# Kernel tuning notes

Measured on AMD Instinct MI355X. Metric: run time of the kernel, lower is better.

## Reference

```python
import jax, jax.numpy as jnp
import numpy as np

B, S, D = 4, 4096, 2048
E, H, SPE = 64, 1024, 1
NUM_SLOTS = E * SPE
TEMP = 1.0


def setup_inputs() -> dict:
    key = jax.random.key(0)
    ks = jax.random.split(key, 6)
    x = jax.random.normal(ks[0], (B, S, D), dtype=jnp.float32)
    W_disp = jax.random.normal(ks[1], (NUM_SLOTS, D), dtype=jnp.float32) * 0.02
    # torch Linear default init ~ U(-1/sqrt(fan_in), 1/sqrt(fan_in))
    W1 = jax.random.uniform(ks[2], (E, H, D), jnp.float32, -1.0, 1.0) / np.sqrt(D)
    b1 = jax.random.uniform(ks[3], (E, H), jnp.float32, -1.0, 1.0) / np.sqrt(D)
    W2 = jax.random.uniform(ks[4], (E, D, H), jnp.float32, -1.0, 1.0) / np.sqrt(H)
    b2 = jax.random.uniform(ks[5], (E, D), jnp.float32, -1.0, 1.0) / np.sqrt(H)
    return {"x": x, "W_disp": W_disp, "W1": W1, "b1": b1, "W2": W2, "b2": b2}


def reference(x, W_disp, W1, b1, W2, b2):
    # eval mode: dropout inactive, no calibration, z_loss_weight=0
    Bb, Ss, Dd = x.shape
    xf = x.reshape(-1, Dd)                       # (T, D)
    logits = (xf @ W_disp.T) / TEMP              # (T, num_slots)
    dispatch = jax.nn.softmax(logits, axis=0)    # softmax over tokens (T > 1)
    combine = jax.nn.softmax(logits, axis=-1)    # softmax over slots
    slot_inputs = dispatch.T @ xf                # (num_slots, D)
    x_exp = slot_inputs.reshape(E, SPE, Dd)      # (E, S_per, D)
    h = jnp.einsum('esd,ehd->esh', x_exp, W1) + b1[:, None, :]
    h = jax.nn.gelu(h, approximate=False)        # torch F.gelu is exact (erf)
    out = jnp.einsum('esh,edh->esd', h, W2) + b2[:, None, :]
    slot_outputs = out.reshape(NUM_SLOTS, Dd)
    y = combine @ slot_outputs                   # (T, D)
    return y.reshape(Bb, Ss, Dd)
```

## Files before the change

kernel.cpp:

```cpp
#include <hip/hip_runtime.h>
#include <math.h>

#define T_TOK 16384
#define D_DIM 2048
#define NSLOT 64
#define H_DIM 1024
#define KSPLIT 8
#define KCH 256
#define TBLK 128

__global__ __launch_bounds__(256) void k_logits(const float* __restrict__ x,
                                                const float* __restrict__ Wd,
                                                float* __restrict__ plog,
                                                float* __restrict__ pz4) {
    __shared__ float xs[128][32];
    __shared__ float ws[64][32];
    const int tid = threadIdx.x;
    if (blockIdx.x == 0 && blockIdx.y == 0) pz4[tid] = 0.f;
    const int tblk = blockIdx.x * TBLK;
    const int koff = blockIdx.y * KCH;
    const int tq = tid >> 3;
    const int sg = tid & 7;
    float acc[4][8] = {};

    for (int kc = 0; kc < KCH; kc += 32) {
        __syncthreads();
        #pragma unroll
        for (int ii = 0; ii < 4; ++ii) {
            int fi = tid + ii * 256; int t = fi >> 3, c = fi & 7;
            *(float4*)&xs[t][(c ^ (t & 7)) << 2] =
                *(const float4*)&x[(size_t)(tblk + t) * D_DIM + koff + kc + c * 4];
        }
        #pragma unroll
        for (int ii = 0; ii < 2; ++ii) {
            int fi = tid + ii * 256; int s = fi >> 3, c = fi & 7;
            *(float4*)&ws[s][(c ^ (s & 7)) << 2] =
                *(const float4*)&Wd[(size_t)s * D_DIM + koff + kc + c * 4];
        }
        __syncthreads();
        #pragma unroll
        for (int c = 0; c < 8; ++c) {
            float4 wv[8];
            #pragma unroll
            for (int j = 0; j < 8; ++j)
                wv[j] = *(const float4*)&ws[sg + 8 * j][(c ^ sg) << 2];
            #pragma unroll
            for (int i = 0; i < 4; ++i) {
                float4 xv = *(const float4*)&xs[tq + 32 * i][(c ^ (tq & 7)) << 2];
                #pragma unroll
                for (int j = 0; j < 8; ++j)
                    acc[i][j] += xv.x * wv[j].x + xv.y * wv[j].y +
                                 xv.z * wv[j].z + xv.w * wv[j].w;
            }
        }
    }
    const size_t ksbase = (size_t)blockIdx.y * T_TOK;
    #pragma unroll
    for (int i = 0; i < 4; ++i)
        #pragma unroll
        for (int j = 0; j < 8; ++j)
            plog[(ksbase + tblk + tq + 32 * i) * NSLOT + sg + 8 * j] = acc[i][j];
}

__global__ __launch_bounds__(256) void k_lsum(const float* __restrict__ plog,
                                              float* __restrict__ elog,
                                              float* __restrict__ pz4) {
    __shared__ float zsh[4][64];
    const int tid = threadIdx.x;
    const int s = tid & 63, rq = tid >> 6;
    const int j0 = blockIdx.x * 32;
    float zacc = 0.f;
    #pragma unroll
    for (int i = 0; i < 8; ++i) {
        int r = j0 + rq * 8 + i;
        float v = 0.f;
        #pragma unroll
        for (int ks = 0; ks < KSPLIT; ++ks)
            v += plog[((size_t)ks * T_TOK + r) * NSLOT + s];
        float e = __expf(v);
        elog[(size_t)r * NSLOT + s] = e;
        zacc += e;
    }
    zsh[rq][s] = zacc;
    __syncthreads();
    if (tid < 64)
        atomicAdd(&pz4[(blockIdx.x & 3) * 64 + tid],
                  zsh[0][tid] + zsh[1][tid] + zsh[2][tid] + zsh[3][tid]);
}

__global__ __launch_bounds__(256) void k_slot(const float* __restrict__ x,
        const float* __restrict__ elog, float* __restrict__ partial) {
    __shared__ float xs[32][256];
    __shared__ float pls[32][64];
    const int tid = threadIdx.x;
    const int d0 = blockIdx.x * 256;
    const int tc0 = blockIdx.y * 256;
    const int dg = tid & 31, sgq = tid >> 5;
    float4 acc0[8] = {}, acc1[8] = {};

    for (int sub = 0; sub < 8; ++sub) {
        const int t0 = tc0 + sub * 32;
        __syncthreads();
        #pragma unroll
        for (int ii = 0; ii < 8; ++ii) {
            int fi = tid + ii * 256; int r = fi >> 6, c4 = fi & 63;
            *(float4*)&xs[r][c4 * 4] =
                *(const float4*)&x[(size_t)(t0 + r) * D_DIM + d0 + c4 * 4];
        }
        #pragma unroll
        for (int ii = 0; ii < 2; ++ii) {
            int fi = tid + ii * 256; int r = fi >> 4, s4 = fi & 15;
            *(float4*)&pls[r][s4 * 4] =
                *(const float4*)&elog[(size_t)(t0 + r) * NSLOT + s4 * 4];
        }
        __syncthreads();
        for (int t = 0; t < 32; ++t) {
            float4 xv0 = *(const float4*)&xs[t][dg * 4];
            float4 xv1 = *(const float4*)&xs[t][128 + dg * 4];
            #pragma unroll
            for (int i = 0; i < 8; ++i) {
                float p = pls[t][sgq * 8 + i];
                acc0[i].x += p * xv0.x; acc0[i].y += p * xv0.y;
                acc0[i].z += p * xv0.z; acc0[i].w += p * xv0.w;
                acc1[i].x += p * xv1.x; acc1[i].y += p * xv1.y;
                acc1[i].z += p * xv1.z; acc1[i].w += p * xv1.w;
            }
        }
    }
    #pragma unroll
    for (int i = 0; i < 8; ++i) {
        int s = sgq * 8 + i;
        *(float4*)&partial[((size_t)blockIdx.y * NSLOT + s) * D_DIM + d0 + dg * 4] = acc0[i];
        *(float4*)&partial[((size_t)blockIdx.y * NSLOT + s) * D_DIM + d0 + 128 + dg * 4] = acc1[i];
    }
}

__global__ __launch_bounds__(256) void k_sred(const float* __restrict__ partial,
                                              const float* __restrict__ pz4,
                                              float* __restrict__ slot_in) {
    const size_t idx = (size_t)blockIdx.x * 256 + threadIdx.x;
    const int s = (int)(idx >> 9);
    const float iz = 1.f / (pz4[s] + pz4[64 + s] + pz4[128 + s] + pz4[192 + s]);
    const float4* p4 = (const float4*)partial;
    float4 a = {0.f, 0.f, 0.f, 0.f};
    for (int c0 = 0; c0 < 8; ++c0) {
        float4 v[8];
        #pragma unroll
        for (int j = 0; j < 8; ++j)
            v[j] = p4[(size_t)(c0 * 8 + j) * (NSLOT * D_DIM / 4) + idx];
        #pragma unroll
        for (int j = 0; j < 8; ++j) {
            a.x += v[j].x; a.y += v[j].y; a.z += v[j].z; a.w += v[j].w;
        }
    }
    a.x *= iz; a.y *= iz; a.z *= iz; a.w *= iz;
    ((float4*)slot_in)[idx] = a;
}

__global__ __launch_bounds__(256) void k_mlp1(const float* __restrict__ W1,
                                              const float* __restrict__ b1,
                                              const float* __restrict__ slot_in,
                                              float* __restrict__ h) {
    const int wave = threadIdx.x >> 6, lane = threadIdx.x & 63;
    const int row = blockIdx.x * 4 + wave;
    const int e = row >> 10;
    const float* wr = W1 + (size_t)row * D_DIM;
    const float* xr = slot_in + (size_t)e * D_DIM;
    float acc = 0.f;
    #pragma unroll
    for (int i = 0; i < 8; ++i) {
        int k = (lane + i * 64) * 4;
        float4 w4 = *(const float4*)(wr + k);
        float4 x4 = *(const float4*)(xr + k);
        acc += w4.x * x4.x + w4.y * x4.y + w4.z * x4.z + w4.w * x4.w;
    }
    #pragma unroll
    for (int off = 32; off; off >>= 1) acc += __shfl_xor(acc, off);
    if (lane == 0) {
        float v = acc + b1[row];
        h[row] = 0.5f * v * (1.f + erff(v * 0.70710678118654752f));
    }
}

__global__ __launch_bounds__(256) void k_mlp2(const float* __restrict__ W2,
                                              const float* __restrict__ b2,
                                              const float* __restrict__ h,
                                              float* __restrict__ slot_out) {
    const int wave = threadIdx.x >> 6, lane = threadIdx.x & 63;
    const int row = blockIdx.x * 4 + wave;
    const int e = row >> 11;
    const float* wr = W2 + (size_t)row * H_DIM;
    const float* xr = h + (size_t)e * H_DIM;
    float acc = 0.f;
    #pragma unroll
    for (int i = 0; i < 4; ++i) {
        int k = (lane + i * 64) * 4;
        float4 w4 = *(const float4*)(wr + k);
        float4 x4 = *(const float4*)(xr + k);
        acc += w4.x * x4.x + w4.y * x4.y + w4.z * x4.z + w4.w * x4.w;
    }
    #pragma unroll
    for (int off = 32; off; off >>= 1) acc += __shfl_xor(acc, off);
    if (lane == 0) slot_out[row] = acc + b2[row];
}

__global__ __launch_bounds__(256) void k_combine(const float* __restrict__ elog,
                                                 const float* __restrict__ so,
                                                 float* __restrict__ y) {
    __shared__ float cl[128][68];
    __shared__ float sol[64][128];
    __shared__ float rinv[128];
    const int tid = threadIdx.x;
    const int d0 = blockIdx.x * 128;
    const int tb = blockIdx.y * 128;
    const int tq = tid >> 4;
    const int dgq = tid & 15;
    #pragma unroll
    for (int ii = 0; ii < 8; ++ii) {
        int fi = tid + ii * 256; int r = fi >> 4, s4 = fi & 15;
        *(float4*)&cl[r][s4 * 4] =
            *(const float4*)&elog[(size_t)(tb + r) * NSLOT + s4 * 4];
    }
    #pragma unroll
    for (int ii = 0; ii < 8; ++ii) {
        int fi = tid + ii * 256; int r = fi >> 5, c4 = fi & 31;
        *(float4*)&sol[r][c4 * 4] =
            *(const float4*)&so[(size_t)r * D_DIM + d0 + c4 * 4];
    }
    __syncthreads();
    if (tid < 128) {
        float zs = 0.f;
        #pragma unroll
        for (int q = 0; q < 16; ++q) {
            float4 v = *(const float4*)&cl[tid][q * 4];
            zs += v.x + v.y + v.z + v.w;
        }
        rinv[tid] = 1.f / zs;
    }
    __syncthreads();
    float4 acc0[8] = {}, acc1[8] = {};
    for (int s = 0; s < 64; ++s) {
        float4 sv0 = *(const float4*)&sol[s][dgq * 4];
        float4 sv1 = *(const float4*)&sol[s][64 + dgq * 4];
        #pragma unroll
        for (int i = 0; i < 8; ++i) {
            float cv = cl[tq + 16 * i][s];
            acc0[i].x += cv * sv0.x; acc0[i].y += cv * sv0.y;
            acc0[i].z += cv * sv0.z; acc0[i].w += cv * sv0.w;
            acc1[i].x += cv * sv1.x; acc1[i].y += cv * sv1.y;
            acc1[i].z += cv * sv1.z; acc1[i].w += cv * sv1.w;
        }
    }
    #pragma unroll
    for (int i = 0; i < 8; ++i) {
        float rz = rinv[tq + 16 * i];
        acc0[i].x *= rz; acc0[i].y *= rz; acc0[i].z *= rz; acc0[i].w *= rz;
        acc1[i].x *= rz; acc1[i].y *= rz; acc1[i].z *= rz; acc1[i].w *= rz;
        *(float4*)&y[(size_t)(tb + tq + 16 * i) * D_DIM + d0 + dgq * 4] = acc0[i];
        *(float4*)&y[(size_t)(tb + tq + 16 * i) * D_DIM + d0 + 64 + dgq * 4] = acc1[i];
    }
}

extern "C" void kernel_launch(void* const* d_in, const int* in_sizes, int n_in,
                              void* d_out, int out_size, void* d_ws, size_t ws_size,
                              hipStream_t stream) {
    const float* x  = (const float*)d_in[0];
    const float* Wd = (const float*)d_in[1];
    const float* W1 = (const float*)d_in[2];
    const float* b1 = (const float*)d_in[3];
    const float* W2 = (const float*)d_in[4];
    const float* b2 = (const float*)d_in[5];
    float* y = (float*)d_out;

    float* w = (float*)d_ws;
    float* plog     = w;
    float* elog     = plog + (size_t)KSPLIT * T_TOK * NSLOT;
    float* pz4      = elog + (size_t)T_TOK * NSLOT;
    float* partial  = pz4 + 256;
    float* slot_in  = partial + (size_t)64 * NSLOT * D_DIM;
    float* h        = slot_in + (size_t)NSLOT * D_DIM;
    float* slot_out = h + (size_t)NSLOT * H_DIM;

    k_logits<<<dim3(T_TOK / TBLK, KSPLIT), 256, 0, stream>>>(x, Wd, plog, pz4);
    k_lsum<<<512, 256, 0, stream>>>(plog, elog, pz4);
    k_slot<<<dim3(8, 64), 256, 0, stream>>>(x, elog, partial);
    k_sred<<<128, 256, 0, stream>>>(partial, pz4, slot_in);
    k_mlp1<<<(NSLOT * H_DIM) / 4, 256, 0, stream>>>(W1, b1, slot_in, h);
    k_mlp2<<<(NSLOT * D_DIM) / 4, 256, 0, stream>>>(W2, b2, h, slot_out);
    k_combine<<<dim3(16, 128), 256, 0, stream>>>(elog, slot_out, y);
}
```

Baseline: 446.9 us.

## Prefetch next tile into registers in logits and slot-reduction kernels

Both the logits GEMM and the slot-input accumulation kernels now load the next tile from global memory into registers while computing on the current shared-memory tile, then write it to shared memory after a barrier. The logits kernel also doubles its K chunk per stage to 64, which halves the number of stages. The aim is to hide global load latency behind FMA work. In exchange it raises register pressure and shared memory use, which may reduce occupancy.

```diff
diff --git a/kernel.cpp b/kernel.cpp
--- a/kernel.cpp
+++ b/kernel.cpp
@@ -13,8 +13,8 @@
                                                 const float* __restrict__ Wd,
                                                 float* __restrict__ plog,
                                                 float* __restrict__ pz4) {
-    __shared__ float xs[128][32];
-    __shared__ float ws[64][32];
+    __shared__ float xs[128 * 64];
+    __shared__ float ws[64 * 64];
     const int tid = threadIdx.x;
     if (blockIdx.x == 0 && blockIdx.y == 0) pz4[tid] = 0.f;
     const int tblk = blockIdx.x * TBLK;
@@ -22,38 +22,66 @@
     const int tq = tid >> 3;
     const int sg = tid & 7;
     float acc[4][8] = {};
-
-    for (int kc = 0; kc < KCH; kc += 32) {
-        __syncthreads();
-        #pragma unroll
-        for (int ii = 0; ii < 4; ++ii) {
-            int fi = tid + ii * 256; int t = fi >> 3, c = fi & 7;
-            *(float4*)&xs[t][(c ^ (t & 7)) << 2] =
-                *(const float4*)&x[(size_t)(tblk + t) * D_DIM + koff + kc + c * 4];
-        }
-        #pragma unroll
-        for (int ii = 0; ii < 2; ++ii) {
-            int fi = tid + ii * 256; int s = fi >> 3, c = fi & 7;
-            *(float4*)&ws[s][(c ^ (s & 7)) << 2] =
-                *(const float4*)&Wd[(size_t)s * D_DIM + koff + kc + c * 4];
-        }
-        __syncthreads();
-        #pragma unroll
-        for (int c = 0; c < 8; ++c) {
+    float4 px[8], pw[4];
+
+    const int xt = tid >> 4, xc = tid & 15;
+
+#define LOADSTAGE(KST)                                                        \
+    {                                                                         \
+        const int kb = koff + (KST) * 64;                                     \
+        _Pragma("unroll")                                                     \
+        for (int ii = 0; ii < 8; ++ii)                                        \
+            px[ii] = *(const float4*)&x[(size_t)(tblk + xt + ii * 16) * D_DIM \
+                                        + kb + xc * 4];                       \
+        _Pragma("unroll")                                                     \
+        for (int ii = 0; ii < 4; ++ii)                                        \
+            pw[ii] = *(const float4*)&Wd[(size_t)(xt + ii * 16) * D_DIM       \
+                                         + kb + xc * 4];                      \
+    }
+
+#define WRITESTAGE()                                                          \
+    {                                                                         \
+        _Pragma("unroll")                                                     \
+        for (int ii = 0; ii < 8; ++ii) {                                      \
+            int t = xt + ii * 16;                                             \
+            *(float4*)&xs[t * 64 + ((xc ^ (t & 7)) << 2)] = px[ii];           \
+        }                                                                     \
+        _Pragma("unroll")                                                     \
+        for (int ii = 0; ii < 4; ++ii) {                                      \
+            int s = xt + ii * 16;                                             \
+            *(float4*)&ws[s * 64 + ((xc ^ (s & 7)) << 2)] = pw[ii];           \
+        }                                                                     \
+    }
+
+    LOADSTAGE(0);
+    WRITESTAGE();
+    __syncthreads();
+    for (int kst = 0; kst < 4; ++kst) {
+        if (kst < 3) LOADSTAGE(kst + 1);
+        #pragma unroll
+        for (int c = 0; c < 16; ++c) {
             float4 wv[8];
             #pragma unroll
             for (int j = 0; j < 8; ++j)
-                wv[j] = *(const float4*)&ws[sg + 8 * j][(c ^ sg) << 2];
+                wv[j] = *(const float4*)&ws[(sg + 8 * j) * 64 + ((c ^ sg) << 2)];
             #pragma unroll
             for (int i = 0; i < 4; ++i) {
-                float4 xv = *(const float4*)&xs[tq + 32 * i][(c ^ (tq & 7)) << 2];
+                float4 xv = *(const float4*)&xs[(tq + 32 * i) * 64
+                                                + ((c ^ (tq & 7)) << 2)];
                 #pragma unroll
                 for (int j = 0; j < 8; ++j)
                     acc[i][j] += xv.x * wv[j].x + xv.y * wv[j].y +
                                  xv.z * wv[j].z + xv.w * wv[j].w;
             }
         }
-    }
+        if (kst < 3) {
+            __syncthreads();
+            WRITESTAGE();
+            __syncthreads();
+        }
+    }
+#undef LOADSTAGE
+#undef WRITESTAGE
     const size_t ksbase = (size_t)blockIdx.y * T_TOK;
     #pragma unroll
     for (int i = 0; i < 4; ++i)
@@ -96,24 +124,39 @@
     const int d0 = blockIdx.x * 256;
     const int tc0 = blockIdx.y * 256;
     const int dg = tid & 31, sgq = tid >> 5;
+    const int xr = tid >> 6, xc = tid & 63;
+    const int pr = tid >> 4, pc = tid & 15;
     float4 acc0[8] = {}, acc1[8] = {};
-
+    float4 gx[8], gp[2];
+
+#define SLOADSTAGE(SUB)                                                       \
+    {                                                                         \
+        const int t0 = tc0 + (SUB) * 32;                                      \
+        _Pragma("unroll")                                                     \
+        for (int ii = 0; ii < 8; ++ii)                                        \
+            gx[ii] = *(const float4*)&x[(size_t)(t0 + xr + ii * 4) * D_DIM    \
+                                        + d0 + xc * 4];                       \
+        _Pragma("unroll")                                                     \
+        for (int ii = 0; ii < 2; ++ii)                                        \
+            gp[ii] = *(const float4*)&elog[(size_t)(t0 + pr + ii * 16)        \
+                                           * NSLOT + pc * 4];                 \
+    }
+
+#define SWRITESTAGE()                                                         \
+    {                                                                         \
+        _Pragma("unroll")                                                     \
+        for (int ii = 0; ii < 8; ++ii)                                        \
+            *(float4*)&xs[xr + ii * 4][xc * 4] = gx[ii];                      \
+        _Pragma("unroll")                                                     \
+        for (int ii = 0; ii < 2; ++ii)                                        \
+            *(float4*)&pls[pr + ii * 16][pc * 4] = gp[ii];                    \
+    }
+
+    SLOADSTAGE(0);
+    SWRITESTAGE();
+    __syncthreads();
     for (int sub = 0; sub < 8; ++sub) {
-        const int t0 = tc0 + sub * 32;
-        __syncthreads();
-        #pragma unroll
-        for (int ii = 0; ii < 8; ++ii) {
-            int fi = tid + ii * 256; int r = fi >> 6, c4 = fi & 63;
-            *(float4*)&xs[r][c4 * 4] =
-                *(const float4*)&x[(size_t)(t0 + r) * D_DIM + d0 + c4 * 4];
-        }
-        #pragma unroll
-        for (int ii = 0; ii < 2; ++ii) {
-            int fi = tid + ii * 256; int r = fi >> 4, s4 = fi & 15;
-            *(float4*)&pls[r][s4 * 4] =
-                *(const float4*)&elog[(size_t)(t0 + r) * NSLOT + s4 * 4];
-        }
-        __syncthreads();
+        if (sub < 7) SLOADSTAGE(sub + 1);
         for (int t = 0; t < 32; ++t) {
             float4 xv0 = *(const float4*)&xs[t][dg * 4];
             float4 xv1 = *(const float4*)&xs[t][128 + dg * 4];
@@ -126,7 +169,14 @@
                 acc1[i].z += p * xv1.z; acc1[i].w += p * xv1.w;
             }
         }
-    }
+        if (sub < 7) {
+            __syncthreads();
+            SWRITESTAGE();
+            __syncthreads();
+        }
+    }
+#undef SLOADSTAGE
+#undef SWRITESTAGE
     #pragma unroll
     for (int i = 0; i < 8; ++i) {
         int s = sgq * 8 + i;
```

Result: slower. 1.053 ms (+135.7%).

## Rebalance grid sizes: split sred reduction, more lsum blocks, persistent-style MLP waves

Applied to the files above, without the earlier changes.

k_lsum now handles 16 rows per block with twice as many blocks, giving more parallelism. k_sred splits the 64-way partial reduction across four waves per block and finishes it in shared memory, raising the grid from 128 to 512 blocks so more CUs pull memory bandwidth. The MLP GEMV kernels switch to a fixed 2048-block grid, with each wave looping over rows strided by 8192, which cuts block launch overhead. The cost is an extra sync and a shared-memory step in sred, plus less latency hiding in the MLP kernels if too few waves stay resident.

```diff
diff --git a/kernel.cpp b/kernel.cpp
--- a/kernel.cpp
+++ b/kernel.cpp
@@ -68,11 +68,11 @@
     __shared__ float zsh[4][64];
     const int tid = threadIdx.x;
     const int s = tid & 63, rq = tid >> 6;
-    const int j0 = blockIdx.x * 32;
+    const int j0 = blockIdx.x * 16;
     float zacc = 0.f;
     #pragma unroll
-    for (int i = 0; i < 8; ++i) {
-        int r = j0 + rq * 8 + i;
+    for (int i = 0; i < 4; ++i) {
+        int r = j0 + rq * 4 + i;
         float v = 0.f;
         #pragma unroll
         for (int ks = 0; ks < KSPLIT; ++ks)
@@ -138,23 +138,37 @@
 __global__ __launch_bounds__(256) void k_sred(const float* __restrict__ partial,
                                               const float* __restrict__ pz4,
                                               float* __restrict__ slot_in) {
-    const size_t idx = (size_t)blockIdx.x * 256 + threadIdx.x;
-    const int s = (int)(idx >> 9);
-    const float iz = 1.f / (pz4[s] + pz4[64 + s] + pz4[128 + s] + pz4[192 + s]);
+    __shared__ float4 red[256];
+    const int tid = threadIdx.x;
+    const int o = blockIdx.x * 64 + (tid & 63);
+    const int part = tid >> 6;
     const float4* p4 = (const float4*)partial;
     float4 a = {0.f, 0.f, 0.f, 0.f};
-    for (int c0 = 0; c0 < 8; ++c0) {
+    #pragma unroll
+    for (int c0 = 0; c0 < 2; ++c0) {
         float4 v[8];
         #pragma unroll
         for (int j = 0; j < 8; ++j)
-            v[j] = p4[(size_t)(c0 * 8 + j) * (NSLOT * D_DIM / 4) + idx];
+            v[j] = p4[(size_t)(part * 16 + c0 * 8 + j) * (NSLOT * D_DIM / 4) + o];
         #pragma unroll
         for (int j = 0; j < 8; ++j) {
             a.x += v[j].x; a.y += v[j].y; a.z += v[j].z; a.w += v[j].w;
         }
     }
-    a.x *= iz; a.y *= iz; a.z *= iz; a.w *= iz;
-    ((float4*)slot_in)[idx] = a;
+    red[tid] = a;
+    __syncthreads();
+    if (tid < 64) {
+        const int s = o >> 9;
+        const float iz = 1.f / (pz4[s] + pz4[64 + s] + pz4[128 + s] + pz4[192 + s]);
+        float4 b = red[tid];
+        #pragma unroll
+        for (int p = 1; p < 4; ++p) {
+            float4 v = red[tid + p * 64];
+            b.x += v.x; b.y += v.y; b.z += v.z; b.w += v.w;
+        }
+        b.x *= iz; b.y *= iz; b.z *= iz; b.w *= iz;
+        ((float4*)slot_in)[o] = b;
+    }
 }
 
 __global__ __launch_bounds__(256) void k_mlp1(const float* __restrict__ W1,
@@ -162,23 +176,26 @@
                                               const float* __restrict__ slot_in,
                                               float* __restrict__ h) {
     const int wave = threadIdx.x >> 6, lane = threadIdx.x & 63;
-    const int row = blockIdx.x * 4 + wave;
-    const int e = row >> 10;
-    const float* wr = W1 + (size_t)row * D_DIM;
-    const float* xr = slot_in + (size_t)e * D_DIM;
-    float acc = 0.f;
-    #pragma unroll
-    for (int i = 0; i < 8; ++i) {
-        int k = (lane + i * 64) * 4;
-        float4 w4 = *(const float4*)(wr + k);
-        float4 x4 = *(const float4*)(xr + k);
-        acc += w4.x * x4.x + w4.y * x4.y + w4.z * x4.z + w4.w * x4.w;
-    }
-    #pragma unroll
-    for (int off = 32; off; off >>= 1) acc += __shfl_xor(acc, off);
-    if (lane == 0) {
-        float v = acc + b1[row];
-        h[row] = 0.5f * v * (1.f + erff(v * 0.70710678118654752f));
+    const int wid = blockIdx.x * 4 + wave;
+    for (int it = 0; it < 8; ++it) {
+        const int row = wid + 8192 * it;
+        const int e = row >> 10;
+        const float* wr = W1 + (size_t)row * D_DIM;
+        const float* xr = slot_in + (size_t)e * D_DIM;
+        float acc = 0.f;
+        #pragma unroll
+        for (int i = 0; i < 8; ++i) {
+            int k = (lane + i * 64) * 4;
+            float4 w4 = *(const float4*)(wr + k);
+            float4 x4 = *(const float4*)(xr + k);
+            acc += w4.x * x4.x + w4.y * x4.y + w4.z * x4.z + w4.w * x4.w;
+        }
+        #pragma unroll
+        for (int off = 32; off; off >>= 1) acc += __shfl_xor(acc, off);
+        if (lane == 0) {
+            float v = acc + b1[row];
+            h[row] = 0.5f * v * (1.f + erff(v * 0.70710678118654752f));
+        }
     }
 }
 
@@ -187,21 +204,24 @@
                                               const float* __restrict__ h,
                                               float* __restrict__ slot_out) {
     const int wave = threadIdx.x >> 6, lane = threadIdx.x & 63;
-    const int row = blockIdx.x * 4 + wave;
-    const int e = row >> 11;
-    const float* wr = W2 + (size_t)row * H_DIM;
-    const float* xr = h + (size_t)e * H_DIM;
-    float acc = 0.f;
-    #pragma unroll
-    for (int i = 0; i < 4; ++i) {
-        int k = (lane + i * 64) * 4;
-        float4 w4 = *(const float4*)(wr + k);
-        float4 x4 = *(const float4*)(xr + k);
-        acc += w4.x * x4.x + w4.y * x4.y + w4.z * x4.z + w4.w * x4.w;
-    }
-    #pragma unroll
-    for (int off = 32; off; off >>= 1) acc += __shfl_xor(acc, off);
-    if (lane == 0) slot_out[row] = acc + b2[row];
+    const int wid = blockIdx.x * 4 + wave;
+    for (int it = 0; it < 16; ++it) {
+        const int row = wid + 8192 * it;
+        const int e = row >> 11;
+        const float* wr = W2 + (size_t)row * H_DIM;
+        const float* xr = h + (size_t)e * H_DIM;
+        float acc = 0.f;
+        #pragma unroll
+        for (int i = 0; i < 4; ++i) {
+            int k = (lane + i * 64) * 4;
+            float4 w4 = *(const float4*)(wr + k);
+            float4 x4 = *(const float4*)(xr + k);
+            acc += w4.x * x4.x + w4.y * x4.y + w4.z * x4.z + w4.w * x4.w;
+        }
+        #pragma unroll
+        for (int off = 32; off; off >>= 1) acc += __shfl_xor(acc, off);
+        if (lane == 0) slot_out[row] = acc + b2[row];
+    }
 }
 
 __global__ __launch_bounds__(256) void k_combine(const float* __restrict__ elog,
@@ -282,10 +302,10 @@
     float* slot_out = h + (size_t)NSLOT * H_DIM;
 
     k_logits<<<dim3(T_TOK / TBLK, KSPLIT), 256, 0, stream>>>(x, Wd, plog, pz4);
-    k_lsum<<<512, 256, 0, stream>>>(plog, elog, pz4);
+    k_lsum<<<1024, 256, 0, stream>>>(plog, elog, pz4);
     k_slot<<<dim3(8, 64), 256, 0, stream>>>(x, elog, partial);
-    k_sred<<<128, 256, 0, stream>>>(partial, pz4, slot_in);
-    k_mlp1<<<(NSLOT * H_DIM) / 4, 256, 0, stream>>>(W1, b1, slot_in, h);
-    k_mlp2<<<(NSLOT * D_DIM) / 4, 256, 0, stream>>>(W2, b2, h, slot_out);
+    k_sred<<<512, 256, 0, stream>>>(partial, pz4, slot_in);
+    k_mlp1<<<2048, 256, 0, stream>>>(W1, b1, slot_in, h);
+    k_mlp2<<<2048, 256, 0, stream>>>(W2, b2, h, slot_out);
     k_combine<<<dim3(16, 128), 256, 0, stream>>>(elog, slot_out, y);
 }
```

Measured after the change: 476.3 us. 1.07x slower.
